# Optimization experiments

Hardware: AMD Instinct MI355X
Metric: run time of the kernel (lower is better)

The kernel has to match this reference:

```python
import jax, jax.numpy as jnp
import numpy as np

THETA = 10000.0
CLASS_RANGE = 24
CLASS_INTERVAL = 4
ROPE_H1 = (0.0, float(CLASS_INTERVAL))                       # (0, 4)
ROPE_H2 = (float(CLASS_RANGE - CLASS_INTERVAL), float(CLASS_RANGE))  # (20, 24)
ROPE_BAK = CLASS_RANGE // 2                                  # 12
EPS = 1e-8


def normalize_and_scale(v, src, tgt):
    s_min, s_max = src
    t_min, t_max = tgt
    return (v - s_min) / (s_max - s_min + EPS) * (t_max - t_min) + t_min


def rope_1d(x, positions):
    # x: (B, H, S, D); positions: (S,)
    D = x.shape[-1]
    inv_freq = 1.0 / (THETA ** (jnp.arange(0, D, 2, dtype=jnp.float32) / D))
    f = positions[:, None] * inv_freq[None, :]          # (S, D/2)
    cos, sin = jnp.cos(f), jnp.sin(f)
    x1, x2 = x[..., 0::2], x[..., 1::2]
    o1 = x1 * cos - x2 * sin
    o2 = x1 * sin + x2 * cos
    return jnp.stack([o1, o2], axis=-1).reshape(x.shape)


def setup_inputs() -> dict:
    key = jax.random.key(0)
    ks = jax.random.split(key, 10)
    B, N_t, S, C = 1, 21, 1560, 2048
    N_a, A = 32, 768
    return {
        "x": jax.random.normal(ks[0], (B, N_t * S, C), jnp.float32),
        "encoder_hidden_states": jax.random.normal(ks[1], (B * N_t, N_a, A), jnp.float32),
        "x_ref_attn_map": jax.random.uniform(ks[2], (2, N_t * S), jnp.float32),
        "q_w": jax.random.normal(ks[3], (C, C), jnp.float32) * 0.02,
        "q_b": jax.random.normal(ks[4], (C,), jnp.float32) * 0.02,
        "kv_w": jax.random.normal(ks[5], (2 * C, A), jnp.float32) * 0.02,
        "kv_b": jax.random.normal(ks[6], (2 * C,), jnp.float32) * 0.02,
        "proj_w": jax.random.normal(ks[7], (C, C), jnp.float32) * 0.02,
        "proj_b": jax.random.normal(ks[8], (C,), jnp.float32) * 0.02,
        "N_t": 21,
    }


def reference(x, encoder_hidden_states, x_ref_attn_map, q_w, q_b, kv_w, kv_b, proj_w, proj_b, N_t):
    B, N_total, C = x.shape
    S = N_total // N_t
    H = 32
    D = C // H
    BNt = B * N_t

    # q projection: (B*N_t, S, H, D)
    xr = x.reshape(BNt, S, C)
    q = (jnp.einsum('bsc,oc->bso', xr, q_w) + q_b).reshape(BNt, S, H, D)

    # multi-person RoPE positions for queries
    h1_max, h1_min = x_ref_attn_map[0].max(), x_ref_attn_map[0].min()
    h2_max, h2_min = x_ref_attn_map[1].max(), x_ref_attn_map[1].min()
    human1 = normalize_and_scale(x_ref_attn_map[0], (h1_min, h1_max), ROPE_H1)
    human2 = normalize_and_scale(x_ref_attn_map[1], (h2_min, h2_max), ROPE_H2)
    back = jnp.full((x_ref_attn_map.shape[1],), ROPE_BAK, dtype=human1.dtype)
    max_idx = jnp.argmax(x_ref_attn_map, axis=0)         # (N_t*S,), values in {0,1}
    nmap = jnp.stack([human1, human2, back], axis=1)     # (N_t*S, 3)
    normalized_pos = jnp.take_along_axis(nmap, max_idx[:, None], axis=1)[:, 0]

    qf = q.reshape(B, N_t * S, H, D).transpose(0, 2, 1, 3)   # (B, H, N_t*S, D)
    qf = rope_1d(qf, normalized_pos)
    q = qf.transpose(0, 2, 1, 3).reshape(BNt, S, H, D)

    # kv projection: (B*N_t, N_a, 2, H, D)
    N_a = encoder_hidden_states.shape[1]
    kv = jnp.einsum('bac,oc->bao', encoder_hidden_states, kv_w) + kv_b
    kv = kv.reshape(BNt, N_a, 2, H, D)
    k, v = kv[:, :, 0], kv[:, :, 1]

    # k RoPE with per-half constant positions
    half = N_a // 2
    per_frame = jnp.concatenate([
        jnp.full((half,), (ROPE_H1[0] + ROPE_H1[1]) / 2, jnp.float32),
        jnp.full((N_a - half,), (ROPE_H2[0] + ROPE_H2[1]) / 2, jnp.float32),
    ])
    encoder_pos = jnp.tile(per_frame, N_t)
    kf = k.reshape(B, N_t * N_a, H, D).transpose(0, 2, 1, 3)
    kf = rope_1d(kf, encoder_pos)
    k = kf.transpose(0, 2, 1, 3).reshape(BNt, N_a, H, D)

    # per-frame windowed cross-attention (non-causal)
    scale = 1.0 / jnp.sqrt(jnp.asarray(D, jnp.float32))
    scores = jnp.einsum('bshd,bahd->bhsa', q, k) * scale     # (BNt, H, S, N_a)
    probs = jax.nn.softmax(scores, axis=-1)
    out = jnp.einsum('bhsa,bahd->bshd', probs, v)            # (BNt, S, H, D)

    out = out.reshape(BNt, S, C)
    out = jnp.einsum('bsc,oc->bso', out, proj_w) + proj_b
    return out.reshape(B, N_t * S, C)
```

## Files before the change

### kernel.cpp

```cpp
#include <hip/hip_runtime.h>

typedef short bf16x8 __attribute__((ext_vector_type(8)));
typedef float f32x4 __attribute__((ext_vector_type(4)));

#define LN10000_32 0.2878231406211853f

__device__ __forceinline__ unsigned short f2bf(float f) {
  union { float f; unsigned int u; } v; v.f = f;
  unsigned int r = v.u + 0x7fffu + ((v.u >> 16) & 1u);
  return (unsigned short)(r >> 16);
}
__device__ __forceinline__ float bf2f(unsigned short h) {
  union { unsigned int u; float f; } v; v.u = ((unsigned int)h) << 16;
  return v.f;
}

__device__ __forceinline__ void stage16(const unsigned short* g, unsigned short* lds_base, int lane) {
#if __has_builtin(__builtin_amdgcn_global_load_lds)
  (void)lane;
  __builtin_amdgcn_global_load_lds((const __attribute__((address_space(1))) void*)g,
                                   (__attribute__((address_space(3))) void*)lds_base,
                                   16, 0, 0);
#else
  *(bf16x8*)((char*)lds_base + lane * 16) = *(const bf16x8*)g;
#endif
}

__global__ void minmax_kernel(const float* __restrict__ xmap, float* __restrict__ mm) {
  __shared__ float red[4][256];
  int t = threadIdx.x;
  float mn0 = 3.4e38f, mx0 = -3.4e38f, mn1 = 3.4e38f, mx1 = -3.4e38f;
  for (int i = t; i < 32760; i += 256) {
    float a = xmap[i];          mn0 = fminf(mn0, a); mx0 = fmaxf(mx0, a);
    float b = xmap[32760 + i];  mn1 = fminf(mn1, b); mx1 = fmaxf(mx1, b);
  }
  red[0][t] = mn0; red[1][t] = mx0; red[2][t] = mn1; red[3][t] = mx1;
  __syncthreads();
  for (int s = 128; s > 0; s >>= 1) {
    if (t < s) {
      red[0][t] = fminf(red[0][t], red[0][t + s]);
      red[1][t] = fmaxf(red[1][t], red[1][t + s]);
      red[2][t] = fminf(red[2][t], red[2][t + s]);
      red[3][t] = fmaxf(red[3][t], red[3][t + s]);
    }
    __syncthreads();
  }
  if (t == 0) { mm[0] = red[0][0]; mm[1] = red[1][0]; mm[2] = red[2][0]; mm[3] = red[3][0]; }
}

__global__ void pos_table_kernel(const float* __restrict__ xmap, const float* __restrict__ mm,
                                 float2* __restrict__ tab) {
  int n = blockIdx.x * 256 + threadIdx.x;
  if (n >= 32760) return;
  float m0 = xmap[n], m1 = xmap[32760 + n];
  float pos;
  if (m1 > m0) pos = (m1 - mm[2]) / (mm[3] - mm[2] + 1e-8f) * 4.0f + 20.0f;
  else         pos = (m0 - mm[0]) / (mm[1] - mm[0] + 1e-8f) * 4.0f;
  #pragma unroll
  for (int j = 0; j < 32; j++) {
    float invf = __expf(-(float)j * LN10000_32);
    float f = pos * invf;
    float s, c;
    sincosf(f, &s, &c);
    tab[(long)n * 32 + j] = make_float2(c, s);
  }
}

__global__ void cast_x_kernel(const float* __restrict__ src, unsigned short* __restrict__ dst) {
  int r = blockIdx.x;
  int c = threadIdx.x * 8;
  bf16x8 o;
  if (r < 32760) {
    const float4* s = (const float4*)(src + (long)r * 2048 + c);
    float4 a = s[0], b = s[1];
    o[0] = (short)f2bf(a.x); o[1] = (short)f2bf(a.y); o[2] = (short)f2bf(a.z); o[3] = (short)f2bf(a.w);
    o[4] = (short)f2bf(b.x); o[5] = (short)f2bf(b.y); o[6] = (short)f2bf(b.z); o[7] = (short)f2bf(b.w);
  } else {
    #pragma unroll
    for (int t = 0; t < 8; t++) o[t] = 0;
  }
  *(bf16x8*)(dst + (long)r * 2048 + c) = o;
}

__global__ void cast_flat_kernel(const float* __restrict__ src, unsigned short* __restrict__ dst, long n8) {
  long i = (long)blockIdx.x * 256 + threadIdx.x;
  if (i >= n8) return;
  const float4* s = (const float4*)(src + i * 8);
  float4 a = s[0], b = s[1];
  bf16x8 o;
  o[0] = (short)f2bf(a.x); o[1] = (short)f2bf(a.y); o[2] = (short)f2bf(a.z); o[3] = (short)f2bf(a.w);
  o[4] = (short)f2bf(b.x); o[5] = (short)f2bf(b.y); o[6] = (short)f2bf(b.z); o[7] = (short)f2bf(b.w);
  *(bf16x8*)(dst + i * 8) = o;
}

__global__ void cast_ehs_kernel(const float* __restrict__ src, unsigned short* __restrict__ dst) {
  int idx = blockIdx.x * 256 + threadIdx.x;
  int r = idx / 96, c = (idx % 96) * 8;
  bf16x8 o;
  if (r < 672) {
    const float4* s = (const float4*)(src + (long)r * 768 + c);
    float4 a = s[0], b = s[1];
    o[0] = (short)f2bf(a.x); o[1] = (short)f2bf(a.y); o[2] = (short)f2bf(a.z); o[3] = (short)f2bf(a.w);
    o[4] = (short)f2bf(b.x); o[5] = (short)f2bf(b.y); o[6] = (short)f2bf(b.z); o[7] = (short)f2bf(b.w);
  } else {
    #pragma unroll
    for (int t = 0; t < 8; t++) o[t] = 0;
  }
  *(bf16x8*)(dst + (long)r * 768 + c) = o;
}

template <int OUTF>
__global__ __launch_bounds__(256, 2)
void gemm_bt(const unsigned short* __restrict__ A, const unsigned short* __restrict__ B,
             const float* __restrict__ bias, void* __restrict__ C,
             int M, int N, int K, int M_valid) {
  __shared__ unsigned short As[128 * 32];
  __shared__ unsigned short Bs[128 * 32];
  int mt = blockIdx.x, nt = blockIdx.y;
  const int m0 = mt * 128;
  const int n0 = nt * 128;
  const int tid = threadIdx.x;
  const int wave = tid >> 6;
  const int lane = tid & 63;
  const int wr = wave >> 1, wc = wave & 1;
  const int lrow = lane >> 2, lcol = lane & 3;

  f32x4 acc[4][4];
  #pragma unroll
  for (int i = 0; i < 4; i++)
    #pragma unroll
    for (int j = 0; j < 4; j++) acc[i][j] = (f32x4){0.f, 0.f, 0.f, 0.f};

  const unsigned short* gA = A + (long)(m0 + wave * 32 + lrow) * K + lcol * 8;
  const unsigned short* gB = B + (long)(n0 + wave * 32 + lrow) * K + lcol * 8;
  unsigned short* lA0 = &As[wave * 1024];
  unsigned short* lA1 = &As[wave * 1024 + 512];
  unsigned short* lB0 = &Bs[wave * 1024];
  unsigned short* lB1 = &Bs[wave * 1024 + 512];

  for (int k0 = 0; k0 < K; k0 += 32) {
    stage16(gA + k0, lA0, lane);
    stage16(gA + k0 + 16 * K, lA1, lane);
    stage16(gB + k0, lB0, lane);
    stage16(gB + k0 + 16 * K, lB1, lane);
    __syncthreads();
    bf16x8 af[4], bfr[4];
    const int kq = (lane >> 4) * 8;
    const int rr = lane & 15;
    #pragma unroll
    for (int mi = 0; mi < 4; mi++) af[mi] = *(const bf16x8*)&As[(wr * 64 + mi * 16 + rr) * 32 + kq];
    #pragma unroll
    for (int ni = 0; ni < 4; ni++) bfr[ni] = *(const bf16x8*)&Bs[(wc * 64 + ni * 16 + rr) * 32 + kq];
    #pragma unroll
    for (int mi = 0; mi < 4; mi++)
      #pragma unroll
      for (int ni = 0; ni < 4; ni++)
        acc[mi][ni] = __builtin_amdgcn_mfma_f32_16x16x32_bf16(af[mi], bfr[ni], acc[mi][ni], 0, 0, 0);
    __syncthreads();
  }

  const int colL = lane & 15, rq = (lane >> 4) * 4;
  #pragma unroll
  for (int mi = 0; mi < 4; mi++) {
    #pragma unroll
    for (int ni = 0; ni < 4; ni++) {
      int col = n0 + wc * 64 + ni * 16 + colL;
      float bv = bias[col];
      #pragma unroll
      for (int r = 0; r < 4; r++) {
        int row = m0 + wr * 64 + mi * 16 + rq + r;
        if (row < M_valid) {
          float v = acc[mi][ni][r] + bv;
          if (OUTF) ((float*)C)[(long)row * N + col] = v;
          else      ((unsigned short*)C)[(long)row * N + col] = f2bf(v);
        }
      }
    }
  }
}

template <int OUTF>
__global__ __launch_bounds__(512, 2)
void gemm256(const unsigned short* __restrict__ A, const unsigned short* __restrict__ B,
             const float* __restrict__ bias, void* __restrict__ C,
             int K, int N, int M_valid) {
  extern __shared__ __align__(16) unsigned short lds[];
  const int NT = K >> 6;
  const int NI = NT >> 1;
  const int orig = blockIdx.x;
  const int cpx = (int)gridDim.x >> 3;
  const int wgid = (orig & 7) * cpx + (orig >> 3);
  const int nt = wgid & 7;
  const int mt = wgid >> 3;
  const int m0 = mt << 8, n0 = nt << 8;
  const int tid = threadIdx.x;
  const int w = tid >> 6, l = tid & 63;
  const int wr = w >> 2, wc = w & 3;
  const int i = l & 15, kq = l >> 4;

  const int swz0 = ((kq) ^ (i & 7)) * 8;
  const int swz1 = ((4 + kq) ^ (i & 7)) * 8;
  const int aoff = wr * 8192 + i * 64;
  const int boff = 16384 + (wc >> 1) * 8192 + (wc & 1) * 4096 + i * 64;

  const int srow = l >> 3;
  const int scb = ((l & 7) ^ srow) * 8;
  const int sdst = w * 512;
  const unsigned short* Asrc = A + (long)(m0 + w * 8 + srow) * K + scb;
  const unsigned short* Bsrc = B + (long)(n0 + w * 8 + srow) * K + scb;

  f32x4 acc[8][4];
  #pragma unroll
  for (int a_ = 0; a_ < 8; a_++)
    #pragma unroll
    for (int b_ = 0; b_ < 4; b_++) acc[a_][b_] = (f32x4){0.f, 0.f, 0.f, 0.f};

  bf16x8 a[4][2], b[4][2];

#define BAR __builtin_amdgcn_s_barrier()
#define VM4 asm volatile("s_waitcnt vmcnt(4)" ::: "memory")
#define VM0 asm volatile("s_waitcnt vmcnt(0)" ::: "memory")

#define STG_A(T, h) do { \
    const unsigned short* s_ = Asrc + (long)((h) * 128) * K + (T) * 64; \
    unsigned short* d_ = lds + (((T) & 1) << 15) + ((h) << 13) + sdst; \
    stage16(s_, d_, l); \
    stage16(s_ + (long)64 * K, d_ + 4096, l); \
  } while (0)
#define STG_B(T, h) do { \
    const unsigned short* s_ = Bsrc + (long)((h) * 128) * K + (T) * 64; \
    unsigned short* d_ = lds + (((T) & 1) << 15) + 16384 + ((h) << 13) + sdst; \
    stage16(s_, d_, l); \
    stage16(s_ + (long)64 * K, d_ + 4096, l); \
  } while (0)

#define RD_A(bufo, mh) do { \
    const unsigned short* p_ = lds + (bufo) + aoff + (mh) * 4096; \
    a[0][0] = *(const bf16x8*)(p_ + swz0);        a[0][1] = *(const bf16x8*)(p_ + swz1); \
    a[1][0] = *(const bf16x8*)(p_ + 1024 + swz0); a[1][1] = *(const bf16x8*)(p_ + 1024 + swz1); \
    a[2][0] = *(const bf16x8*)(p_ + 2048 + swz0); a[2][1] = *(const bf16x8*)(p_ + 2048 + swz1); \
    a[3][0] = *(const bf16x8*)(p_ + 3072 + swz0); a[3][1] = *(const bf16x8*)(p_ + 3072 + swz1); \
  } while (0)
#define RD_B(bufo, nf) do { \
    const unsigned short* p_ = lds + (bufo) + boff + (nf) * 1024; \
    b[nf][0] = *(const bf16x8*)(p_ + swz0); \
    b[nf][1] = *(const bf16x8*)(p_ + swz1); \
  } while (0)

#define MMQ(AB, N0, N1) do { \
    __builtin_amdgcn_s_setprio(1); \
    _Pragma("unroll") \
    for (int q_ = 0; q_ < 4; q_++) { \
      acc[(AB) + q_][N0] = __builtin_amdgcn_mfma_f32_16x16x32_bf16(a[q_][0], b[N0][0], acc[(AB) + q_][N0], 0, 0, 0); \
      acc[(AB) + q_][N1] = __builtin_amdgcn_mfma_f32_16x16x32_bf16(a[q_][0], b[N1][0], acc[(AB) + q_][N1], 0, 0, 0); \
    } \
    _Pragma("unroll") \
    for (int q_ = 0; q_ < 4; q_++) { \
      acc[(AB) + q_][N0] = __builtin_amdgcn_mfma_f32_16x16x32_bf16(a[q_][1], b[N0][1], acc[(AB) + q_][N0], 0, 0, 0); \
      acc[(AB) + q_][N1] = __builtin_amdgcn_mfma_f32_16x16x32_bf16(a[q_][1], b[N1][1], acc[(AB) + q_][N1], 0, 0, 0); \
    } \
    __builtin_amdgcn_s_setprio(0); \
  } while (0)

#define GEMM_ITER(T0v, T1v, FULL, GATEP4, GATEP8) do { \
    const int T0_ = (T0v), T1_ = (T1v); \
     RD_A(0, 0); RD_B(0, 0); RD_B(0, 1); STG_B(T1_, 1); BAR; MMQ(0, 0, 1); BAR; \
     RD_B(0, 2); RD_B(0, 3); STG_A(T1_, 1); BAR; MMQ(0, 2, 3); BAR; \
     RD_A(0, 1); if (FULL) { STG_B(T0_ + 2, 0); } BAR; MMQ(4, 2, 3); BAR; \
     if (FULL) { STG_A(T0_ + 2, 0); } GATEP4; BAR; MMQ(4, 0, 1); BAR; \
     RD_A(32768, 0); RD_B(32768, 0); RD_B(32768, 1); if (FULL) { STG_B(T0_ + 2, 1); } BAR; MMQ(0, 0, 1); BAR; \
     RD_B(32768, 2); RD_B(32768, 3); if (FULL) { STG_A(T0_ + 2, 1); } BAR; MMQ(0, 2, 3); BAR; \
     RD_A(32768, 1); if (FULL) { STG_B(T1_ + 2, 0); } BAR; MMQ(4, 2, 3); BAR; \
     if (FULL) { STG_A(T1_ + 2, 0); } GATEP8; BAR; MMQ(4, 0, 1); BAR; \
  } while (0)

  STG_B(0, 0); STG_A(0, 0); STG_B(0, 1); STG_A(0, 1);
  STG_B(1, 0); STG_A(1, 0);
  VM4; BAR;

  for (int j = 0; j < NI - 1; ++j) {
    GEMM_ITER(2 * j, 2 * j + 1, 1, VM4, VM4);
  }
  GEMM_ITER(NT - 2, NT - 1, 0, VM0, (void)0);

#undef GEMM_ITER
#undef MMQ
#undef RD_B
#undef RD_A
#undef STG_B
#undef STG_A
#undef VM0
#undef VM4
#undef BAR

  #pragma unroll
  for (int nf = 0; nf < 4; nf++) {
    int col = n0 + wc * 64 + nf * 16 + i;
    float bv = bias[col];
    #pragma unroll
    for (int mf = 0; mf < 8; mf++) {
      int rowb = m0 + wr * 128 + mf * 16 + kq * 4;
      #pragma unroll
      for (int r = 0; r < 4; r++) {
        int row = rowb + r;
        if (row < M_valid) {
          float v = acc[mf][nf][r] + bv;
          if (OUTF) ((float*)C)[(long)row * N + col] = v;
          else      ((unsigned short*)C)[(long)row * N + col] = f2bf(v);
        }
      }
    }
  }
}

__global__ void rope_k_kernel(unsigned short* __restrict__ kv) {
  int r = blockIdx.x;
  int c = threadIdx.x * 8;
  float pos = ((r & 31) < 16) ? 2.0f : 22.0f;
  unsigned short* p = kv + (long)r * 4096 + c;
  bf16x8 v = *(const bf16x8*)p;
  int jb = (c & 63) >> 1;
  bf16x8 o;
  #pragma unroll
  for (int t = 0; t < 4; t++) {
    float invf = __expf(-(float)(jb + t) * LN10000_32);
    float f = pos * invf;
    float s_, c_;
    sincosf(f, &s_, &c_);
    float x1 = bf2f((unsigned short)v[2 * t]);
    float x2 = bf2f((unsigned short)v[2 * t + 1]);
    o[2 * t]     = (short)f2bf(x1 * c_ - x2 * s_);
    o[2 * t + 1] = (short)f2bf(x1 * s_ + x2 * c_);
  }
  *(bf16x8*)p = o;
}

__global__ __launch_bounds__(256)
void attn_kernel(const unsigned short* __restrict__ kv, unsigned short* __restrict__ q,
                 const float2* __restrict__ tab) {
  __shared__ float Ks[2048];
  __shared__ float Vs[2048];
  const int bh = blockIdx.y;
  const int b = bh >> 5, h = bh & 31;
  const int tid = threadIdx.x;
  for (int i = tid; i < 2048; i += 256) {
    int a = i >> 6, d = i & 63;
    long off = ((long)(b * 32 + a)) * 4096 + h * 64 + d;
    Ks[i] = bf2f(kv[off]);
    Vs[i] = bf2f(kv[off + 2048]);
  }
  __syncthreads();
  int s = blockIdx.x * 256 + tid;
  if (s >= 1560) return;
  const long row = (long)b * 1560 + s;
  unsigned short* qp = q + row * 2048 + h * 64;
  float qr[64];
  #pragma unroll
  for (int i = 0; i < 8; i++) {
    bf16x8 v = *(const bf16x8*)(qp + i * 8);
    #pragma unroll
    for (int j = 0; j < 8; j++) qr[i * 8 + j] = bf2f((unsigned short)v[j]);
  }
  const float2* trow = tab + row * 32;
  #pragma unroll
  for (int j = 0; j < 32; j++) {
    float2 cs = trow[j];
    float x1 = qr[2 * j], x2 = qr[2 * j + 1];
    qr[2 * j]     = x1 * cs.x - x2 * cs.y;
    qr[2 * j + 1] = x1 * cs.y + x2 * cs.x;
  }
  float sc[32];
  float mx = -3.4e38f;
  #pragma unroll
  for (int a = 0; a < 32; a++) {
    float acc = 0.f;
    #pragma unroll
    for (int d = 0; d < 64; d++) acc = fmaf(qr[d], Ks[a * 64 + d], acc);
    acc *= 0.125f;
    sc[a] = acc;
    mx = fmaxf(mx, acc);
  }
  float sum = 0.f;
  #pragma unroll
  for (int a = 0; a < 32; a++) { float e = __expf(sc[a] - mx); sc[a] = e; sum += e; }
  float inv = 1.f / sum;
  float outr[64];
  #pragma unroll
  for (int d = 0; d < 64; d++) outr[d] = 0.f;
  #pragma unroll
  for (int a = 0; a < 32; a++) {
    float p = sc[a] * inv;
    #pragma unroll
    for (int d = 0; d < 64; d++) outr[d] = fmaf(p, Vs[a * 64 + d], outr[d]);
  }
  #pragma unroll
  for (int i = 0; i < 8; i++) {
    bf16x8 v;
    #pragma unroll
    for (int j = 0; j < 8; j++) v[j] = (short)f2bf(outr[i * 8 + j]);
    *(bf16x8*)(qp + i * 8) = v;
  }
}

extern "C" void kernel_launch(void* const* d_in, const int* in_sizes, int n_in,
                              void* d_out, int out_size, void* d_ws, size_t ws_size,
                              hipStream_t stream) {
  const float* x      = (const float*)d_in[0];
  const float* ehs    = (const float*)d_in[1];
  const float* xmap   = (const float*)d_in[2];
  const float* q_w    = (const float*)d_in[3];
  const float* q_b    = (const float*)d_in[4];
  const float* kv_w   = (const float*)d_in[5];
  const float* kv_b   = (const float*)d_in[6];
  const float* proj_w = (const float*)d_in[7];
  const float* proj_b = (const float*)d_in[8];
  float* out = (float*)d_out;

  char* ws = (char*)d_ws;
  float*          mm    = (float*)(ws + 0);
  float2*         tab   = (float2*)(ws + 256);
  unsigned short* qbuf  = (unsigned short*)(ws + 8388864);
  unsigned short* kvbuf = (unsigned short*)(ws + 142606592);
  unsigned short* ehsb  = (unsigned short*)(ws + 148898048);
  unsigned short* qwb   = (unsigned short*)(ws + 150077696);
  unsigned short* kvwb  = (unsigned short*)(ws + 158466304);
  unsigned short* pwb   = (unsigned short*)(ws + 164757760);
  unsigned short* xb    = (unsigned short*)d_out;

  (void)hipFuncSetAttribute((const void*)gemm256<0>, hipFuncAttributeMaxDynamicSharedMemorySize, 131072);
  (void)hipFuncSetAttribute((const void*)gemm256<1>, hipFuncAttributeMaxDynamicSharedMemorySize, 131072);

  minmax_kernel<<<1, 256, 0, stream>>>(xmap, mm);
  pos_table_kernel<<<128, 256, 0, stream>>>(xmap, mm, tab);
  cast_x_kernel<<<32768, 256, 0, stream>>>(x, xb);
  cast_flat_kernel<<<2048, 256, 0, stream>>>(q_w, qwb, 524288);
  cast_flat_kernel<<<1536, 256, 0, stream>>>(kv_w, kvwb, 393216);
  cast_flat_kernel<<<2048, 256, 0, stream>>>(proj_w, pwb, 524288);
  cast_ehs_kernel<<<288, 256, 0, stream>>>(ehs, ehsb);

  gemm256<0><<<1024, 512, 131072, stream>>>(xb, qwb, q_b, qbuf, 2048, 2048, 32768);
  gemm_bt<0><<<dim3(6, 32), 256, 0, stream>>>(ehsb, kvwb, kv_b, kvbuf, 768, 4096, 768, 768);

  rope_k_kernel<<<672, 256, 0, stream>>>(kvbuf);

  attn_kernel<<<dim3(7, 672), 256, 0, stream>>>(kvbuf, qbuf, tab);

  gemm256<1><<<1024, 512, 131072, stream>>>(qbuf, pwb, proj_b, out, 2048, 2048, 32760);
}
```

Before: 1.048 ms.

## Restructure 256x256 GEMM main loop into k-half phased register/LDS pipeline

Rewrites the gemm256 inner loop so each 64-wide K tile is split into two 32-wide halves. Each wave holds separate A/B fragment registers per half and issues 16 MFMAs per phase. A and B staging is now issued as whole 256-row tiles at different points in the schedule, and the next buffer's first fragments are prefetched before the last MFMA phase. The aim is to overlap LDS reads and global-to-LDS loads with MFMA work more evenly. In exchange it uses more fragment registers and adds a full vmcnt(0) wait inside every tile, which may stall on outstanding loads.

```diff
diff --git a/kernel.cpp b/kernel.cpp
--- a/kernel.cpp
+++ b/kernel.cpp
@@ -186,7 +186,6 @@
              int K, int N, int M_valid) {
   extern __shared__ __align__(16) unsigned short lds[];
   const int NT = K >> 6;
-  const int NI = NT >> 1;
   const int orig = blockIdx.x;
   const int cpx = (int)gridDim.x >> 3;
   const int wgid = (orig & 7) * cpx + (orig >> 3);
@@ -198,16 +197,14 @@
   const int wr = w >> 2, wc = w & 3;
   const int i = l & 15, kq = l >> 4;
 
-  const int swz0 = ((kq) ^ (i & 7)) * 8;
-  const int swz1 = ((4 + kq) ^ (i & 7)) * 8;
-  const int aoff = wr * 8192 + i * 64;
-  const int boff = 16384 + (wc >> 1) * 8192 + (wc & 1) * 4096 + i * 64;
-
-  const int srow = l >> 3;
-  const int scb = ((l & 7) ^ srow) * 8;
+  const int sw0 = ((kq ^ (i & 7)) << 3);
+  const int sw1 = (((4 + kq) ^ (i & 7)) << 3);
+  const int sA = wr * 8192 + i * 64;
+  const int sB = 16384 + (wc >> 1) * 8192 + (wc & 1) * 4096 + i * 64;
+
   const int sdst = w * 512;
-  const unsigned short* Asrc = A + (long)(m0 + w * 8 + srow) * K + scb;
-  const unsigned short* Bsrc = B + (long)(n0 + w * 8 + srow) * K + scb;
+  const unsigned short* Asrc = A + (long)(m0 + w * 8 + (l >> 3)) * K + (((l & 7) ^ (l >> 3)) << 3);
+  const unsigned short* Bsrc = B + (long)(n0 + w * 8 + (l >> 3)) * K + (((l & 7) ^ (l >> 3)) << 3);
 
   f32x4 acc[8][4];
   #pragma unroll
@@ -215,82 +212,90 @@
     #pragma unroll
     for (int b_ = 0; b_ < 4; b_++) acc[a_][b_] = (f32x4){0.f, 0.f, 0.f, 0.f};
 
-  bf16x8 a[4][2], b[4][2];
+  bf16x8 a00[4], a10[4], a11[4], a01[4];
+  bf16x8 b0[4], b1[4];
 
 #define BAR __builtin_amdgcn_s_barrier()
+#define VM0 asm volatile("s_waitcnt vmcnt(0)" ::: "memory")
 #define VM4 asm volatile("s_waitcnt vmcnt(4)" ::: "memory")
-#define VM0 asm volatile("s_waitcnt vmcnt(0)" ::: "memory")
-
-#define STG_A(T, h) do { \
-    const unsigned short* s_ = Asrc + (long)((h) * 128) * K + (T) * 64; \
-    unsigned short* d_ = lds + (((T) & 1) << 15) + ((h) << 13) + sdst; \
-    stage16(s_, d_, l); \
-    stage16(s_ + (long)64 * K, d_ + 4096, l); \
-  } while (0)
-#define STG_B(T, h) do { \
-    const unsigned short* s_ = Bsrc + (long)((h) * 128) * K + (T) * 64; \
-    unsigned short* d_ = lds + (((T) & 1) << 15) + 16384 + ((h) << 13) + sdst; \
-    stage16(s_, d_, l); \
-    stage16(s_ + (long)64 * K, d_ + 4096, l); \
-  } while (0)
-
-#define RD_A(bufo, mh) do { \
-    const unsigned short* p_ = lds + (bufo) + aoff + (mh) * 4096; \
-    a[0][0] = *(const bf16x8*)(p_ + swz0);        a[0][1] = *(const bf16x8*)(p_ + swz1); \
-    a[1][0] = *(const bf16x8*)(p_ + 1024 + swz0); a[1][1] = *(const bf16x8*)(p_ + 1024 + swz1); \
-    a[2][0] = *(const bf16x8*)(p_ + 2048 + swz0); a[2][1] = *(const bf16x8*)(p_ + 2048 + swz1); \
-    a[3][0] = *(const bf16x8*)(p_ + 3072 + swz0); a[3][1] = *(const bf16x8*)(p_ + 3072 + swz1); \
-  } while (0)
-#define RD_B(bufo, nf) do { \
-    const unsigned short* p_ = lds + (bufo) + boff + (nf) * 1024; \
-    b[nf][0] = *(const bf16x8*)(p_ + swz0); \
-    b[nf][1] = *(const bf16x8*)(p_ + swz1); \
-  } while (0)
-
-#define MMQ(AB, N0, N1) do { \
+
+#define RDA(dst, BUF, mh, SW) do { \
+    const unsigned short* p_ = lds + (BUF) + sA + (mh) * 4096 + (SW); \
+    dst[0] = *(const bf16x8*)(p_); \
+    dst[1] = *(const bf16x8*)(p_ + 1024); \
+    dst[2] = *(const bf16x8*)(p_ + 2048); \
+    dst[3] = *(const bf16x8*)(p_ + 3072); \
+  } while (0)
+#define RDB(dst, BUF, SW) do { \
+    const unsigned short* p_ = lds + (BUF) + sB + (SW); \
+    dst[0] = *(const bf16x8*)(p_); \
+    dst[1] = *(const bf16x8*)(p_ + 1024); \
+    dst[2] = *(const bf16x8*)(p_ + 2048); \
+    dst[3] = *(const bf16x8*)(p_ + 3072); \
+  } while (0)
+
+#define STGA(T, BUF) do { \
+    const unsigned short* s_ = Asrc + (long)(T) * 64; \
+    stage16(s_,                lds + (BUF) + sdst, l); \
+    stage16(s_ + (long)64 * K, lds + (BUF) + 4096 + sdst, l); \
+    stage16(s_ + (long)128 * K, lds + (BUF) + 8192 + sdst, l); \
+    stage16(s_ + (long)192 * K, lds + (BUF) + 12288 + sdst, l); \
+  } while (0)
+#define STGB(T, BUF) do { \
+    const unsigned short* s_ = Bsrc + (long)(T) * 64; \
+    stage16(s_,                lds + (BUF) + 16384 + sdst, l); \
+    stage16(s_ + (long)64 * K, lds + (BUF) + 20480 + sdst, l); \
+    stage16(s_ + (long)128 * K, lds + (BUF) + 24576 + sdst, l); \
+    stage16(s_ + (long)192 * K, lds + (BUF) + 28672 + sdst, l); \
+  } while (0)
+
+#define MM(mh, A_, B_) do { \
     __builtin_amdgcn_s_setprio(1); \
     _Pragma("unroll") \
     for (int q_ = 0; q_ < 4; q_++) { \
-      acc[(AB) + q_][N0] = __builtin_amdgcn_mfma_f32_16x16x32_bf16(a[q_][0], b[N0][0], acc[(AB) + q_][N0], 0, 0, 0); \
-      acc[(AB) + q_][N1] = __builtin_amdgcn_mfma_f32_16x16x32_bf16(a[q_][0], b[N1][0], acc[(AB) + q_][N1], 0, 0, 0); \
-    } \
-    _Pragma("unroll") \
-    for (int q_ = 0; q_ < 4; q_++) { \
-      acc[(AB) + q_][N0] = __builtin_amdgcn_mfma_f32_16x16x32_bf16(a[q_][1], b[N0][1], acc[(AB) + q_][N0], 0, 0, 0); \
-      acc[(AB) + q_][N1] = __builtin_amdgcn_mfma_f32_16x16x32_bf16(a[q_][1], b[N1][1], acc[(AB) + q_][N1], 0, 0, 0); \
+      _Pragma("unroll") \
+      for (int n_ = 0; n_ < 4; n_++) \
+        acc[(mh) * 4 + q_][n_] = __builtin_amdgcn_mfma_f32_16x16x32_bf16(A_[q_], B_[n_], acc[(mh) * 4 + q_][n_], 0, 0, 0); \
     } \
     __builtin_amdgcn_s_setprio(0); \
   } while (0)
 
-#define GEMM_ITER(T0v, T1v, FULL, GATEP4, GATEP8) do { \
-    const int T0_ = (T0v), T1_ = (T1v); \
-     RD_A(0, 0); RD_B(0, 0); RD_B(0, 1); STG_B(T1_, 1); BAR; MMQ(0, 0, 1); BAR; \
-     RD_B(0, 2); RD_B(0, 3); STG_A(T1_, 1); BAR; MMQ(0, 2, 3); BAR; \
-     RD_A(0, 1); if (FULL) { STG_B(T0_ + 2, 0); } BAR; MMQ(4, 2, 3); BAR; \
-     if (FULL) { STG_A(T0_ + 2, 0); } GATEP4; BAR; MMQ(4, 0, 1); BAR; \
-     RD_A(32768, 0); RD_B(32768, 0); RD_B(32768, 1); if (FULL) { STG_B(T0_ + 2, 1); } BAR; MMQ(0, 0, 1); BAR; \
-     RD_B(32768, 2); RD_B(32768, 3); if (FULL) { STG_A(T0_ + 2, 1); } BAR; MMQ(0, 2, 3); BAR; \
-     RD_A(32768, 1); if (FULL) { STG_B(T1_ + 2, 0); } BAR; MMQ(4, 2, 3); BAR; \
-     if (FULL) { STG_A(T1_ + 2, 0); } GATEP8; BAR; MMQ(4, 0, 1); BAR; \
-  } while (0)
-
-  STG_B(0, 0); STG_A(0, 0); STG_B(0, 1); STG_A(0, 1);
-  STG_B(1, 0); STG_A(1, 0);
-  VM4; BAR;
-
+#define TILE(BUF, OBUF, TA, DOA, TB, DOB, DON) do { \
+     RDA(a10, BUF, 1, sw0); if (DOA) STGA(TA, OBUF); \
+    BAR; MM(0, a00, b0); BAR; \
+     RDA(a11, BUF, 1, sw1); RDB(b1, BUF, sw1); \
+    BAR; MM(1, a10, b0); BAR; \
+     RDA(a01, BUF, 0, sw1); VM0; \
+    BAR; MM(1, a11, b1); BAR; \
+     if (DON) { RDA(a00, OBUF, 0, sw0); RDB(b0, OBUF, sw0); } \
+    if (DOB) STGB(TB, BUF); \
+    BAR; MM(0, a01, b1); BAR; \
+  } while (0)
+
+  STGA(0, 0); STGB(0, 0);
+  STGB(1, 32768);
+  VM4;
+  BAR;
+  RDA(a00, 0, 0, sw0);
+  RDB(b0, 0, sw0);
+
+  const int NI = NT >> 1;
   for (int j = 0; j < NI - 1; ++j) {
-    GEMM_ITER(2 * j, 2 * j + 1, 1, VM4, VM4);
-  }
-  GEMM_ITER(NT - 2, NT - 1, 0, VM0, (void)0);
-
-#undef GEMM_ITER
-#undef MMQ
-#undef RD_B
-#undef RD_A
-#undef STG_B
-#undef STG_A
+    const int T0 = 2 * j;
+    TILE(0, 32768, T0 + 1, 1, T0 + 2, 1, 1);
+    TILE(32768, 0, T0 + 2, 1, T0 + 3, 1, 1);
+  }
+  TILE(0, 32768, NT - 1, 1, 0, 0, 1);
+  TILE(32768, 0, 0, 0, 0, 0, 0);
+
+#undef TILE
+#undef MM
+#undef STGB
+#undef STGA
+#undef RDB
+#undef RDA
+#undef VM4
 #undef VM0
-#undef VM4
 #undef BAR
 
   #pragma unroll
```

Result: slower. 1.194 ms (+14.0%).

## Rewrite cross-attention with bf16 MFMA and fuse K RoPE into it

Applied to the files above, without the earlier changes.

The scalar per-thread attention kernel, which kept 64-wide q and output vectors in registers and read K/V from shared memory, is replaced by an MFMA-based kernel. Each wave handles 32 query rows, computes QK^T and PV with 16x16x32 bf16 MFMAs, and does the softmax with lane shuffles, staging P and transposed V in LDS. The separate K RoPE kernel is removed and its rotation is done on the fly inside the attention kernel. This cuts one launch and the scalar FMA work. In exchange P is rounded to bf16 before the PV product, and every block recomputes the K rotation.

```diff
diff --git a/kernel.cpp b/kernel.cpp
--- a/kernel.cpp
+++ b/kernel.cpp
@@ -313,92 +313,148 @@
   }
 }
 
-__global__ void rope_k_kernel(unsigned short* __restrict__ kv) {
-  int r = blockIdx.x;
-  int c = threadIdx.x * 8;
-  float pos = ((r & 31) < 16) ? 2.0f : 22.0f;
-  unsigned short* p = kv + (long)r * 4096 + c;
-  bf16x8 v = *(const bf16x8*)p;
-  int jb = (c & 63) >> 1;
-  bf16x8 o;
-  #pragma unroll
-  for (int t = 0; t < 4; t++) {
-    float invf = __expf(-(float)(jb + t) * LN10000_32);
-    float f = pos * invf;
-    float s_, c_;
-    sincosf(f, &s_, &c_);
-    float x1 = bf2f((unsigned short)v[2 * t]);
-    float x2 = bf2f((unsigned short)v[2 * t + 1]);
-    o[2 * t]     = (short)f2bf(x1 * c_ - x2 * s_);
-    o[2 * t + 1] = (short)f2bf(x1 * s_ + x2 * c_);
-  }
-  *(bf16x8*)p = o;
-}
-
 __global__ __launch_bounds__(256)
-void attn_kernel(const unsigned short* __restrict__ kv, unsigned short* __restrict__ q,
-                 const float2* __restrict__ tab) {
-  __shared__ float Ks[2048];
-  __shared__ float Vs[2048];
+void attn_mfma(const unsigned short* __restrict__ kv, unsigned short* __restrict__ q,
+               const float2* __restrict__ tab) {
+  __shared__ unsigned short Vt[64 * 40];
+  __shared__ unsigned short Pl[4][32 * 40];
   const int bh = blockIdx.y;
   const int b = bh >> 5, h = bh & 31;
   const int tid = threadIdx.x;
-  for (int i = tid; i < 2048; i += 256) {
-    int a = i >> 6, d = i & 63;
-    long off = ((long)(b * 32 + a)) * 4096 + h * 64 + d;
-    Ks[i] = bf2f(kv[off]);
-    Vs[i] = bf2f(kv[off + 2048]);
-  }
+  const int w = tid >> 6, l = tid & 63;
+  const int i16 = l & 15, kq = l >> 4;
+
+  {
+    int a = tid & 31, d0 = (tid >> 5) * 8;
+    const unsigned short* vp = kv + ((long)(b * 32 + a)) * 4096 + 2048 + h * 64 + d0;
+    bf16x8 v = *(const bf16x8*)vp;
+    #pragma unroll
+    for (int j = 0; j < 8; j++) Vt[(d0 + j) * 40 + a] = (unsigned short)v[j];
+  }
+
+  bf16x8 bk[2][2];
+  #pragma unroll
+  for (int nf = 0; nf < 2; nf++) {
+    int a = nf * 16 + i16;
+    float pos = (a < 16) ? 2.0f : 22.0f;
+    const unsigned short* kp = kv + ((long)(b * 32 + a)) * 4096 + h * 64;
+    #pragma unroll
+    for (int ks = 0; ks < 2; ks++) {
+      int d0 = ks * 32 + kq * 8;
+      bf16x8 v = *(const bf16x8*)(kp + d0);
+      bf16x8 o;
+      #pragma unroll
+      for (int t = 0; t < 4; t++) {
+        float invf = __expf(-(float)((d0 >> 1) + t) * LN10000_32);
+        float f = pos * invf, s_, c_;
+        sincosf(f, &s_, &c_);
+        float x1 = bf2f((unsigned short)v[2 * t]), x2 = bf2f((unsigned short)v[2 * t + 1]);
+        o[2 * t]     = (short)f2bf(x1 * c_ - x2 * s_);
+        o[2 * t + 1] = (short)f2bf(x1 * s_ + x2 * c_);
+      }
+      bk[nf][ks] = o;
+    }
+  }
+
   __syncthreads();
-  int s = blockIdx.x * 256 + tid;
-  if (s >= 1560) return;
-  const long row = (long)b * 1560 + s;
-  unsigned short* qp = q + row * 2048 + h * 64;
-  float qr[64];
-  #pragma unroll
-  for (int i = 0; i < 8; i++) {
-    bf16x8 v = *(const bf16x8*)(qp + i * 8);
-    #pragma unroll
-    for (int j = 0; j < 8; j++) qr[i * 8 + j] = bf2f((unsigned short)v[j]);
-  }
-  const float2* trow = tab + row * 32;
-  #pragma unroll
-  for (int j = 0; j < 32; j++) {
-    float2 cs = trow[j];
-    float x1 = qr[2 * j], x2 = qr[2 * j + 1];
-    qr[2 * j]     = x1 * cs.x - x2 * cs.y;
-    qr[2 * j + 1] = x1 * cs.y + x2 * cs.x;
-  }
-  float sc[32];
-  float mx = -3.4e38f;
-  #pragma unroll
-  for (int a = 0; a < 32; a++) {
-    float acc = 0.f;
-    #pragma unroll
-    for (int d = 0; d < 64; d++) acc = fmaf(qr[d], Ks[a * 64 + d], acc);
-    acc *= 0.125f;
-    sc[a] = acc;
-    mx = fmaxf(mx, acc);
-  }
-  float sum = 0.f;
-  #pragma unroll
-  for (int a = 0; a < 32; a++) { float e = __expf(sc[a] - mx); sc[a] = e; sum += e; }
-  float inv = 1.f / sum;
-  float outr[64];
-  #pragma unroll
-  for (int d = 0; d < 64; d++) outr[d] = 0.f;
-  #pragma unroll
-  for (int a = 0; a < 32; a++) {
-    float p = sc[a] * inv;
-    #pragma unroll
-    for (int d = 0; d < 64; d++) outr[d] = fmaf(p, Vs[a * 64 + d], outr[d]);
-  }
-  #pragma unroll
-  for (int i = 0; i < 8; i++) {
-    bf16x8 v;
-    #pragma unroll
-    for (int j = 0; j < 8; j++) v[j] = (short)f2bf(outr[i * 8 + j]);
-    *(bf16x8*)(qp + i * 8) = v;
+
+  const int s0 = blockIdx.x * 128 + w * 32;
+  bf16x8 aq[2][2];
+  #pragma unroll
+  for (int mf = 0; mf < 2; mf++) {
+    int srow = s0 + mf * 16 + i16;
+    int sc_ = srow < 1560 ? srow : 1559;
+    long row = (long)b * 1560 + sc_;
+    const unsigned short* qp = q + row * 2048 + h * 64;
+    const float2* trow = tab + row * 32;
+    #pragma unroll
+    for (int ks = 0; ks < 2; ks++) {
+      int d0 = ks * 32 + kq * 8;
+      bf16x8 v = *(const bf16x8*)(qp + d0);
+      float4 t0 = *(const float4*)&trow[(d0 >> 1)];
+      float4 t1 = *(const float4*)&trow[(d0 >> 1) + 2];
+      float cs[4] = {t0.x, t0.z, t1.x, t1.z};
+      float sn[4] = {t0.y, t0.w, t1.y, t1.w};
+      bf16x8 o;
+      #pragma unroll
+      for (int t = 0; t < 4; t++) {
+        float x1 = bf2f((unsigned short)v[2 * t]), x2 = bf2f((unsigned short)v[2 * t + 1]);
+        o[2 * t]     = (short)f2bf(x1 * cs[t] - x2 * sn[t]);
+        o[2 * t + 1] = (short)f2bf(x1 * sn[t] + x2 * cs[t]);
+      }
+      aq[mf][ks] = o;
+    }
+  }
+
+  f32x4 sfr[2][2];
+  #pragma unroll
+  for (int mf = 0; mf < 2; mf++)
+    #pragma unroll
+    for (int nf = 0; nf < 2; nf++) {
+      f32x4 c = {0.f, 0.f, 0.f, 0.f};
+      c = __builtin_amdgcn_mfma_f32_16x16x32_bf16(aq[mf][0], bk[nf][0], c, 0, 0, 0);
+      c = __builtin_amdgcn_mfma_f32_16x16x32_bf16(aq[mf][1], bk[nf][1], c, 0, 0, 0);
+      sfr[mf][nf] = c;
+    }
+
+  float inv_s[2][4];
+  #pragma unroll
+  for (int mf = 0; mf < 2; mf++) {
+    #pragma unroll
+    for (int r = 0; r < 4; r++) {
+      float v0 = sfr[mf][0][r] * 0.125f;
+      float v1 = sfr[mf][1][r] * 0.125f;
+      float mx = fmaxf(v0, v1);
+      #pragma unroll
+      for (int m_ = 1; m_ < 16; m_ <<= 1) mx = fmaxf(mx, __shfl_xor(mx, m_));
+      float e0 = __expf(v0 - mx), e1 = __expf(v1 - mx);
+      float sm = e0 + e1;
+      #pragma unroll
+      for (int m_ = 1; m_ < 16; m_ <<= 1) sm += __shfl_xor(sm, m_);
+      inv_s[mf][r] = 1.0f / sm;
+      sfr[mf][0][r] = e0; sfr[mf][1][r] = e1;
+    }
+  }
+
+  unsigned short* pl = &Pl[w][0];
+  #pragma unroll
+  for (int mf = 0; mf < 2; mf++)
+    #pragma unroll
+    for (int nf = 0; nf < 2; nf++)
+      #pragma unroll
+      for (int r = 0; r < 4; r++)
+        pl[(mf * 16 + kq * 4 + r) * 40 + nf * 16 + i16] = f2bf(sfr[mf][nf][r]);
+
+  bf16x8 pa[2];
+  #pragma unroll
+  for (int mf = 0; mf < 2; mf++)
+    pa[mf] = *(const bf16x8*)&pl[(mf * 16 + i16) * 40 + kq * 8];
+  bf16x8 vb[4];
+  #pragma unroll
+  for (int nf = 0; nf < 4; nf++)
+    vb[nf] = *(const bf16x8*)&Vt[(nf * 16 + i16) * 40 + kq * 8];
+  f32x4 ofr[2][4];
+  #pragma unroll
+  for (int mf = 0; mf < 2; mf++)
+    #pragma unroll
+    for (int nf = 0; nf < 4; nf++) {
+      f32x4 c = {0.f, 0.f, 0.f, 0.f};
+      ofr[mf][nf] = __builtin_amdgcn_mfma_f32_16x16x32_bf16(pa[mf], vb[nf], c, 0, 0, 0);
+    }
+
+  #pragma unroll
+  for (int mf = 0; mf < 2; mf++) {
+    #pragma unroll
+    for (int r = 0; r < 4; r++) {
+      int srow = s0 + mf * 16 + kq * 4 + r;
+      if (srow < 1560) {
+        unsigned short* op = q + ((long)b * 1560 + srow) * 2048 + h * 64;
+        float inv = inv_s[mf][r];
+        #pragma unroll
+        for (int nf = 0; nf < 4; nf++)
+          op[nf * 16 + i16] = f2bf(ofr[mf][nf][r] * inv);
+      }
+    }
   }
 }
 
@@ -441,9 +497,7 @@
   gemm256<0><<<1024, 512, 131072, stream>>>(xb, qwb, q_b, qbuf, 2048, 2048, 32768);
   gemm_bt<0><<<dim3(6, 32), 256, 0, stream>>>(ehsb, kvwb, kv_b, kvbuf, 768, 4096, 768, 768);
 
-  rope_k_kernel<<<672, 256, 0, stream>>>(kvbuf);
-
-  attn_kernel<<<dim3(7, 672), 256, 0, stream>>>(kvbuf, qbuf, tab);
+  attn_mfma<<<dim3(13, 672), 256, 0, stream>>>(kvbuf, qbuf, tab);
 
   gemm256<1><<<1024, 512, 131072, stream>>>(qbuf, pwb, proj_b, out, 2048, 2048, 32760);
 }
```

New measurement: 875.3 us. 16.5% less time.
